# Optimization experiments

Measured on AMD Instinct MI355X. Metric: run time of the kernel, lower is better.

Reference implementation:

```python
import jax, jax.numpy as jnp
import numpy as np

IM_MAX = 1.0
IM_SIZE = 128
N_THRESHOLDS = 64


def _thresholds():
    # end = im_size * sqrt(2) // 2  (float32 math, floor-div) -> 90.0
    end = np.float32(np.float32(IM_SIZE) * np.sqrt(np.float32(2.0))) // np.float32(2.0)
    t = np.linspace(2.0, float(end), N_THRESHOLDS, dtype=np.float32)
    return np.round(t).astype(np.int32)  # half-to-even, matches torch.round


def _masks():
    # stack of circular low-pass masks, one per threshold: [T, H, W]
    crow, ccol = IM_SIZE // 2, IM_SIZE // 2
    y = np.arange(IM_SIZE)[:, None]
    x = np.arange(IM_SIZE)[None, :]
    r2 = (x - ccol) ** 2 + (y - crow) ** 2  # [H, W]
    thr = _thresholds().astype(np.int64)
    m = (r2[None, :, :] <= (thr[:, None, None] ** 2)).astype(np.float32)
    return jnp.asarray(m)


def setup_inputs() -> dict:
    key = jax.random.key(0)
    k1, k2 = jax.random.split(key)
    shape = (256, 3, IM_SIZE, IM_SIZE)
    prediction = jax.random.uniform(k1, shape, dtype=jnp.float32)
    gt = jax.random.uniform(k2, shape, dtype=jnp.float32)
    return {"prediction": prediction, "gt": gt}


def reference(prediction, gt):
    # Single FFT pass on each input (original redundantly recomputes per threshold,
    # but mask is 0/1 so masked-diff energy = mask * |pred_f - gt_f|^2).
    pf = jnp.fft.fftshift(jnp.fft.fft2(prediction), axes=(-2, -1))  # [B,C,H,W] c64
    gf = jnp.fft.fftshift(jnp.fft.fft2(gt), axes=(-2, -1))
    diff = pf - gf
    sq_err = diff.real ** 2 + diff.imag ** 2  # |.|^2, [B,C,H,W] f32
    masks = _masks()  # [T,H,W]
    # sum_sq_error per (batch, threshold): sum over C,H,W with mask
    sum_sq = jnp.einsum('thw,bchw->bt', masks, sq_err)  # [B,T]
    n_pixels = IM_SIZE * IM_SIZE
    const = 20.0 * jnp.log10(jnp.float32(IM_MAX * n_pixels))
    cf_psnr = const - 10.0 * jnp.log10(sum_sq)
    return cf_psnr
```

## Files before the change

### kernel.cpp

```cpp
#include <hip/hip_runtime.h>
#include <hip/hip_fp16.h>

#define IMG 128
#define NPIX (IMG * IMG)
#define NT 64
#define LSU 129
#define ZCH (64 * LSU)

__device__ __constant__ int c_thr[NT] = {
    2, 3, 5, 6, 8, 9, 10, 12, 13, 15, 16, 17, 19, 20, 22, 23,
    24, 26, 27, 29, 30, 31, 33, 34, 36, 37, 38, 40, 41, 43, 44, 45,
    47, 48, 49, 51, 52, 54, 55, 56, 58, 59, 61, 62, 63, 65, 66, 68,
    69, 70, 72, 73, 75, 76, 77, 79, 80, 82, 83, 84, 86, 87, 89, 90};

__device__ __forceinline__ int rev7(int x) { return (int)(__brev((unsigned)x) >> 25); }

__device__ __forceinline__ unsigned packh2(float x, float y) {
    __half2 h = __floats2half2_rn(x, y);
    return *reinterpret_cast<unsigned*>(&h);
}
__device__ __forceinline__ float2 unpackh2(unsigned u) {
    __half2 h;
    *reinterpret_cast<unsigned*>(&h) = u;
    return __half22float2(h);
}

__device__ __forceinline__ float x1f(float v) {
    return __int_as_float(__builtin_amdgcn_mov_dpp(__float_as_int(v), 0xB1, 0xF, 0xF, true));
}
__device__ __forceinline__ float x2f(float v) {
    return __int_as_float(__builtin_amdgcn_mov_dpp(__float_as_int(v), 0x4E, 0xF, 0xF, true));
}
__device__ __forceinline__ float x3f(float v) {
    return __int_as_float(__builtin_amdgcn_mov_dpp(__float_as_int(v), 0x1B, 0xF, 0xF, true));
}
__device__ __forceinline__ float x7f(float v) {
    return __int_as_float(__builtin_amdgcn_mov_dpp(__float_as_int(v), 0x141, 0xF, 0xF, true));
}
__device__ __forceinline__ float x4f(float v) {
    return x7f(x3f(v));
}
__device__ __forceinline__ float x8f(float v) {
    return __int_as_float(__builtin_amdgcn_mov_dpp(__float_as_int(v), 0x128, 0xF, 0xF, true));
}

__global__ __launch_bounds__(1024) void fused_psnr_kernel(const float* __restrict__ pred,
                                                          const float* __restrict__ gt,
                                                          float* __restrict__ out) {
    __shared__ unsigned s_z[3 * ZCH];
    __shared__ float s_h[16][66];
    __shared__ int s_rc2bin[91];

    const int tid = threadIdx.x;
    const int lane = tid & 63;
    const int wave = tid >> 6;
    const int l = lane & 15;
    const int g = lane >> 4;
    const int b = blockIdx.x;

    for (int i = tid; i < 16 * 66; i += 1024) (&s_h[0][0])[i] = 0.0f;
    if (tid < 91) {
        int t = 0;
        while (t < 63 && c_thr[t] < tid) ++t;
        s_rc2bin[tid] = t;
    }

    const float K = -6.2831853071795864769f * (1.0f / 128.0f);
    float c64[4], s64[4], c32[2], s32[2], c16v, s16v;
#pragma unroll
    for (int j = 0; j < 4; ++j) sincosf(K * (float)(16 * j + l), &s64[j], &c64[j]);
    sincosf(K * (float)(2 * l), &s32[0], &c32[0]);
    sincosf(K * (float)(2 * l + 32), &s32[1], &c32[1]);
    sincosf(K * (float)(4 * l), &s16v, &c16v);
    float c8v, s8v, c4v, s4v, c2v, s2v;
    sincosf(K * (float)((l & 8) ? (l & 7) * 8 : 0), &s8v, &c8v);
    sincosf(K * (float)((l & 4) ? (l & 3) * 16 : 0), &s4v, &c4v);
    sincosf(K * (float)((l & 2) ? (l & 1) * 32 : 0), &s2v, &c2v);
    const float sg8 = (l & 8) ? -1.0f : 1.0f;
    const float sg4 = (l & 4) ? -1.0f : 1.0f;
    const float sg2 = (l & 2) ? -1.0f : 1.0f;
    const float sg1 = (l & 1) ? -1.0f : 1.0f;

    auto bfly = [](float& ar, float& ai, float& br, float& bi, float wc, float wsn) {
        const float dr = ar - br, di = ai - bi;
        ar += br; ai += bi;
        br = dr * wc - di * wsn;
        bi = dr * wsn + di * wc;
    };

    auto fft = [&](float* vr, float* vi) {
#pragma unroll
        for (int j = 0; j < 4; ++j) bfly(vr[j], vi[j], vr[j + 4], vi[j + 4], c64[j], s64[j]);
        bfly(vr[0], vi[0], vr[2], vi[2], c32[0], s32[0]);
        bfly(vr[1], vi[1], vr[3], vi[3], c32[1], s32[1]);
        bfly(vr[4], vi[4], vr[6], vi[6], c32[0], s32[0]);
        bfly(vr[5], vi[5], vr[7], vi[7], c32[1], s32[1]);
#pragma unroll
        for (int j = 0; j < 8; j += 2) bfly(vr[j], vi[j], vr[j + 1], vi[j + 1], c16v, s16v);
#pragma unroll
        for (int j = 0; j < 8; ++j) {
            const float pr = x8f(vr[j]), pi = x8f(vi[j]);
            const float xr = fmaf(sg8, vr[j], pr), xi = fmaf(sg8, vi[j], pi);
            vr[j] = xr * c8v - xi * s8v;
            vi[j] = xr * s8v + xi * c8v;
        }
#pragma unroll
        for (int j = 0; j < 8; ++j) {
            const float pr = x4f(vr[j]), pi = x4f(vi[j]);
            const float xr = fmaf(sg4, vr[j], pr), xi = fmaf(sg4, vi[j], pi);
            vr[j] = xr * c4v - xi * s4v;
            vi[j] = xr * s4v + xi * c4v;
        }
#pragma unroll
        for (int j = 0; j < 8; ++j) {
            const float pr = x2f(vr[j]), pi = x2f(vi[j]);
            const float xr = fmaf(sg2, vr[j], pr), xi = fmaf(sg2, vi[j], pi);
            vr[j] = xr * c2v - xi * s2v;
            vi[j] = xr * s2v + xi * c2v;
        }
#pragma unroll
        for (int j = 0; j < 8; ++j) {
            const float pr = x1f(vr[j]), pi = x1f(vi[j]);
            vr[j] = fmaf(sg1, vr[j], pr);
            vi[j] = fmaf(sg1, vi[j], pi);
        }
    };

    const size_t ibase = (size_t)b * 3 * NPIX;

    auto ldRow = [&](int T, float* buf) {
        const int ch = T >> 4;
        const int Bp = T & 15;
        const int q = (Bp & 7) | ((Bp >> 3) << 5);
        const int r = q + 8 * g;
        const float* pe = pred + ibase + (size_t)ch * NPIX + (size_t)(2 * r) * IMG;
        const float* ge = gt + ibase + (size_t)ch * NPIX + (size_t)(2 * r) * IMG;
#pragma unroll
        for (int j = 0; j < 8; ++j) {
            const int o = 16 * j + l;
            buf[j] = pe[o];
            buf[8 + j] = pe[IMG + o];
            buf[16 + j] = ge[o];
            buf[24 + j] = ge[IMG + o];
        }
    };
    auto doRow = [&](int T, const float* buf) {
        const int ch = T >> 4;
        const int Bp = T & 15;
        const int q = (Bp & 7) | ((Bp >> 3) << 5);
        const int r = q + 8 * g;
        float vr[8], vi[8];
#pragma unroll
        for (int j = 0; j < 8; ++j) {
            vr[j] = 0.5f * (buf[j] - buf[16 + j]);
            vi[j] = 0.5f * (buf[8 + j] - buf[24 + j]);
        }
        fft(vr, vi);
        const int zb = ch * ZCH + r * LSU;
#pragma unroll
        for (int j = 0; j < 8; ++j) s_z[zb + 16 * j + l] = packh2(vr[j], vi[j]);
    };

    {
        float bufA[32], bufB[32];
        ldRow(wave, bufA);
        ldRow(16 + wave, bufB);
        doRow(wave, bufA);
        ldRow(32 + wave, bufA);
        doRow(16 + wave, bufB);
        doRow(32 + wave, bufA);
    }
    __syncthreads();

    float dy2f[8];
    const int r4 = ((l & 1) << 3) | ((l & 2) << 1) | ((l & 4) >> 1) | ((l & 8) >> 3);
#pragma unroll
    for (int j = 0; j < 8; ++j) {
        const int fy = (((j & 1) << 2) | (j & 2) | ((j & 4) >> 2)) | (r4 << 3);
        const int dy = (fy < 64) ? fy : 128 - fy;
        dy2f[j] = (float)(dy * dy);
    }
    const int zr = l >> 1;
    const int odd = l & 1;

    auto ldZf = [&](int T, unsigned* raw) {
        const int ch = T / 17;
        const int t = T - ch * 17;
        const int u = (t < 16) ? ((t & 3) + ((t >> 2) << 4) + 4 * g) : 64;
        const int c1 = rev7(u);
        const int c2 = rev7((128 - u) & 127);
        const int zb = ch * ZCH;
#pragma unroll
        for (int j = 0; j < 8; ++j) {
            const int rowo = zb + (8 * j + zr) * LSU;
            raw[2 * j] = s_z[rowo + c1];
            raw[2 * j + 1] = s_z[rowo + c2];
        }
    };
    auto doCol = [&](int T, const unsigned* raw) {
        const int ch = T / 17;
        const int t = T - ch * 17;
        int u;
        float wf;
        if (t < 16) {
            u = (t & 3) + ((t >> 2) << 4) + 4 * g;
            wf = (u == 0) ? 1.0f : 2.0f;
        } else {
            u = 64;
            wf = (g == 0) ? 1.0f : 0.0f;
        }
        float vr[8], vi[8];
#pragma unroll
        for (int j = 0; j < 8; ++j) {
            const float2 A = unpackh2(raw[2 * j]);
            const float2 B = unpackh2(raw[2 * j + 1]);
            vr[j] = odd ? (A.y + B.y) : (A.x + B.x);
            vi[j] = odd ? (B.x - A.x) : (A.y - B.y);
        }
        fft(vr, vi);
        const float u2f = (float)(u * u);
#pragma unroll
        for (int j = 0; j < 8; ++j) {
            const float r2f = dy2f[j] + u2f;
            if (wf != 0.0f && r2f <= 8100.0f) {
                const int rc = (int)ceilf(sqrtf(r2f) - 3e-4f);
                atomicAdd(&s_h[wave][s_rc2bin[rc]], wf * (vr[j] * vr[j] + vi[j] * vi[j]));
            }
        }
    };

    {
        unsigned zA[16], zB[16];
        ldZf(wave, zA);
        ldZf(wave + 16, zB);
        doCol(wave, zA);
        ldZf(wave + 32, zA);
        doCol(wave + 16, zB);
        if (wave + 48 < 51) ldZf(wave + 48, zB);
        doCol(wave + 32, zA);
        if (wave + 48 < 51) doCol(wave + 48, zB);
    }
    __syncthreads();

    if (tid < 64) {
        float tot = 0.0f;
#pragma unroll
        for (int w = 0; w < 16; ++w) tot += s_h[w][tid];
        s_h[0][tid] = tot;
        float cum = 0.0f;
        for (int j = 0; j <= tid; ++j) cum += s_h[0][j];
        out[b * NT + tid] = 84.2883987849f - 10.0f * log10f(cum);
    }
}

extern "C" void kernel_launch(void* const* d_in, const int* in_sizes, int n_in,
                              void* d_out, int out_size, void* d_ws, size_t ws_size,
                              hipStream_t stream) {
    const float* pred = (const float*)d_in[0];
    const float* gt = (const float*)d_in[1];
    float* out = (float*)d_out;
    fused_psnr_kernel<<<256, 1024, 0, stream>>>(pred, gt, out);
}
```

Before: 58.03 us.

## Pipeline per-channel row and column FFTs with double-buffered LDS

Restructures the kernel so each channel's row FFT is written into one of two LDS buffers while the column FFT of the previous channel reads the other. This shrinks shared memory from three channel slabs to two, which may allow better occupancy, and overlaps global loads with column work. In exchange it adds extra block-wide barriers and gives up the earlier interleaved register prefetch of column data. The u=64 column is now handled by a single wave per channel, which concentrates that extra work and adds some load imbalance.

Result: slower. 120.1 us (+107.0%).

```diff
diff --git a/kernel.cpp b/kernel.cpp
--- a/kernel.cpp
+++ b/kernel.cpp
@@ -5,7 +5,7 @@
 #define NPIX (IMG * IMG)
 #define NT 64
 #define LSU 129
-#define ZCH (64 * LSU)
+#define ZN (64 * LSU)
 
 __device__ __constant__ int c_thr[NT] = {
     2, 3, 5, 6, 8, 9, 10, 12, 13, 15, 16, 17, 19, 20, 22, 23,
@@ -37,9 +37,7 @@
 __device__ __forceinline__ float x7f(float v) {
     return __int_as_float(__builtin_amdgcn_mov_dpp(__float_as_int(v), 0x141, 0xF, 0xF, true));
 }
-__device__ __forceinline__ float x4f(float v) {
-    return x7f(x3f(v));
-}
+__device__ __forceinline__ float x4f(float v) { return x7f(x3f(v)); }
 __device__ __forceinline__ float x8f(float v) {
     return __int_as_float(__builtin_amdgcn_mov_dpp(__float_as_int(v), 0x128, 0xF, 0xF, true));
 }
@@ -47,7 +45,7 @@
 __global__ __launch_bounds__(1024) void fused_psnr_kernel(const float* __restrict__ pred,
                                                           const float* __restrict__ gt,
                                                           float* __restrict__ out) {
-    __shared__ unsigned s_z[3 * ZCH];
+    __shared__ unsigned s_z[2][ZN];
     __shared__ float s_h[16][66];
     __shared__ int s_rc2bin[91];
 
@@ -127,14 +125,23 @@
     };
 
     const size_t ibase = (size_t)b * 3 * NPIX;
-
-    auto ldRow = [&](int T, float* buf) {
-        const int ch = T >> 4;
-        const int Bp = T & 15;
-        const int q = (Bp & 7) | ((Bp >> 3) << 5);
-        const int r = q + 8 * g;
-        const float* pe = pred + ibase + (size_t)ch * NPIX + (size_t)(2 * r) * IMG;
-        const float* ge = gt + ibase + (size_t)ch * NPIX + (size_t)(2 * r) * IMG;
+    const int rrow = (wave & 7) + 32 * (wave >> 3) + 8 * g;
+    const int u0 = (wave & 3) + ((wave >> 2) << 4) + 4 * g;
+    const int zr = l >> 1;
+    const int odd = l & 1;
+
+    float dy2f[8];
+    const int r4 = ((l & 1) << 3) | ((l & 2) << 1) | ((l & 4) >> 1) | ((l & 8) >> 3);
+#pragma unroll
+    for (int j = 0; j < 8; ++j) {
+        const int fy = (((j & 1) << 2) | (j & 2) | ((j & 4) >> 2)) | (r4 << 3);
+        const int dy = (fy < 64) ? fy : 128 - fy;
+        dy2f[j] = (float)(dy * dy);
+    }
+
+    auto ldRow = [&](int ch, float* buf) {
+        const float* pe = pred + ibase + (size_t)ch * NPIX + (size_t)(2 * rrow) * IMG;
+        const float* ge = gt + ibase + (size_t)ch * NPIX + (size_t)(2 * rrow) * IMG;
 #pragma unroll
         for (int j = 0; j < 8; ++j) {
             const int o = 16 * j + l;
@@ -144,11 +151,7 @@
             buf[24 + j] = ge[IMG + o];
         }
     };
-    auto doRow = [&](int T, const float* buf) {
-        const int ch = T >> 4;
-        const int Bp = T & 15;
-        const int q = (Bp & 7) | ((Bp >> 3) << 5);
-        const int r = q + 8 * g;
+    auto stRow = [&](const float* buf, unsigned* zb) {
         float vr[8], vi[8];
 #pragma unroll
         for (int j = 0; j < 8; ++j) {
@@ -156,64 +159,18 @@
             vi[j] = 0.5f * (buf[8 + j] - buf[24 + j]);
         }
         fft(vr, vi);
-        const int zb = ch * ZCH + r * LSU;
-#pragma unroll
-        for (int j = 0; j < 8; ++j) s_z[zb + 16 * j + l] = packh2(vr[j], vi[j]);
-    };
-
-    {
-        float bufA[32], bufB[32];
-        ldRow(wave, bufA);
-        ldRow(16 + wave, bufB);
-        doRow(wave, bufA);
-        ldRow(32 + wave, bufA);
-        doRow(16 + wave, bufB);
-        doRow(32 + wave, bufA);
-    }
-    __syncthreads();
-
-    float dy2f[8];
-    const int r4 = ((l & 1) << 3) | ((l & 2) << 1) | ((l & 4) >> 1) | ((l & 8) >> 3);
-#pragma unroll
-    for (int j = 0; j < 8; ++j) {
-        const int fy = (((j & 1) << 2) | (j & 2) | ((j & 4) >> 2)) | (r4 << 3);
-        const int dy = (fy < 64) ? fy : 128 - fy;
-        dy2f[j] = (float)(dy * dy);
-    }
-    const int zr = l >> 1;
-    const int odd = l & 1;
-
-    auto ldZf = [&](int T, unsigned* raw) {
-        const int ch = T / 17;
-        const int t = T - ch * 17;
-        const int u = (t < 16) ? ((t & 3) + ((t >> 2) << 4) + 4 * g) : 64;
+#pragma unroll
+        for (int j = 0; j < 8; ++j) zb[rrow * LSU + 16 * j + l] = packh2(vr[j], vi[j]);
+    };
+    auto colOne = [&](int u, float wf, const unsigned* zb) {
         const int c1 = rev7(u);
         const int c2 = rev7((128 - u) & 127);
-        const int zb = ch * ZCH;
-#pragma unroll
-        for (int j = 0; j < 8; ++j) {
-            const int rowo = zb + (8 * j + zr) * LSU;
-            raw[2 * j] = s_z[rowo + c1];
-            raw[2 * j + 1] = s_z[rowo + c2];
-        }
-    };
-    auto doCol = [&](int T, const unsigned* raw) {
-        const int ch = T / 17;
-        const int t = T - ch * 17;
-        int u;
-        float wf;
-        if (t < 16) {
-            u = (t & 3) + ((t >> 2) << 4) + 4 * g;
-            wf = (u == 0) ? 1.0f : 2.0f;
-        } else {
-            u = 64;
-            wf = (g == 0) ? 1.0f : 0.0f;
-        }
         float vr[8], vi[8];
 #pragma unroll
         for (int j = 0; j < 8; ++j) {
-            const float2 A = unpackh2(raw[2 * j]);
-            const float2 B = unpackh2(raw[2 * j + 1]);
+            const int rowo = (8 * j + zr) * LSU;
+            const float2 A = unpackh2(zb[rowo + c1]);
+            const float2 B = unpackh2(zb[rowo + c2]);
             vr[j] = odd ? (A.y + B.y) : (A.x + B.x);
             vi[j] = odd ? (B.x - A.x) : (A.y - B.y);
         }
@@ -228,18 +185,27 @@
             }
         }
     };
-
-    {
-        unsigned zA[16], zB[16];
-        ldZf(wave, zA);
-        ldZf(wave + 16, zB);
-        doCol(wave, zA);
-        ldZf(wave + 32, zA);
-        doCol(wave + 16, zB);
-        if (wave + 48 < 51) ldZf(wave + 48, zB);
-        doCol(wave + 32, zA);
-        if (wave + 48 < 51) doCol(wave + 48, zB);
-    }
+    auto colPhase = [&](int ch, const unsigned* zb) {
+        colOne(u0, (u0 == 0) ? 1.0f : 2.0f, zb);
+        if (wave == ch) colOne(64, (g == 0) ? 1.0f : 0.0f, zb);
+    };
+
+    float bufA[32], bufB[32];
+    ldRow(0, bufA);
+    stRow(bufA, s_z[0]);
+    __syncthreads();
+
+    ldRow(1, bufB);
+    colPhase(0, s_z[0]);
+    stRow(bufB, s_z[1]);
+    __syncthreads();
+
+    ldRow(2, bufA);
+    colPhase(1, s_z[1]);
+    stRow(bufA, s_z[0]);
+    __syncthreads();
+
+    colPhase(2, s_z[0]);
     __syncthreads();
 
     if (tid < 64) {
```
